# Kernel tuning notes

Hardware: AMD Instinct MI355X
Metric: run time of the kernel (lower is better)

Reference implementation:

```python
import jax, jax.numpy as jnp
import numpy as np

P = 2.0
HARDNESS_RATIO = 0.1
MARGIN = 0.0
EPS = 1e-7

N, DFEAT, NCLS = 4096, 128, 64


def setup_inputs() -> dict:
    key = jax.random.key(0)
    kx, ky = jax.random.split(key)
    x = jax.random.normal(kx, (N, DFEAT), dtype=jnp.float32)
    y = jax.random.randint(ky, (N,), 0, NCLS, dtype=jnp.int64)
    return {"x": x, "y": y}


def reference(x, y):
    # torch.cdist(x, x, p=2) via gram-matrix identity (clamped for sqrt stability)
    sq = jnp.sum(x * x, axis=1)                      # [N]
    D2 = sq[:, None] + sq[None, :] - 2.0 * (x @ x.T)  # [N, N]
    D = jnp.sqrt(jnp.maximum(D2, 1e-12))

    # label agreement masks (no-grad in torch; integer-derived so no float grad anyway)
    agree = (y[None, :] == y[:, None]).astype(x.dtype)   # [N, N]
    disagree = 1.0 - agree
    # With 64 samples/class every row is valid (>=1 positive and >=1 negative),
    # so the torch valid_rows filter keeps all rows; we compute all rows.

    # sort each row by distance, drop self (column 0), gather
    col_idx = jnp.argsort(D, axis=1)[:, 1:]               # [N, N-1]
    dist = jnp.take_along_axis(D, col_idx, axis=1)        # [N, N-1]
    a = jnp.take_along_axis(agree, col_idx, axis=1)
    d = jnp.take_along_axis(disagree, col_idx, axis=1)

    found_agree = jnp.cumsum(a, axis=1)
    found_agree = found_agree / (jnp.sum(found_agree, axis=1, keepdims=True) + EPS)
    found_disagree = jnp.cumsum(d, axis=1)
    found_disagree = found_disagree / (jnp.sum(found_disagree, axis=1, keepdims=True) + EPS)

    negative_hardness = jax.lax.stop_gradient(d * (found_disagree / (found_agree + HARDNESS_RATIO)))
    positive_hardness = jax.lax.stop_gradient(a * ((found_disagree + HARDNESS_RATIO) / (found_agree + HARDNESS_RATIO)))

    per_sample_score = jnp.mean(
        jax.nn.relu(dist * positive_hardness + MARGIN - dist * negative_hardness), axis=1
    )  # [N]

    sample_performance = jnp.sum(found_agree - found_disagree, axis=1)
    sample_performance = sample_performance - jnp.min(sample_performance)
    sample_weight = jax.lax.stop_gradient(1.0 / (sample_performance + 1.0))
    return per_sample_score * sample_weight
```

## Files before the change

### kernel.cpp

```cpp
#include <hip/hip_runtime.h>
#include <math.h>
#include <float.h>


#define N 4096
#define DF 128
#define NCLS 64
#define MAXP 128
#define TSTR 128
#define DSTR 128
#define NB 256
#define HPAD 260
#define BSCALE 0.5f

typedef __bf16 bf16x8 __attribute__((ext_vector_type(8)));
typedef float f32x4 __attribute__((ext_vector_type(4)));
typedef unsigned int u32x4 __attribute__((ext_vector_type(4)));

static __device__ __forceinline__ unsigned short f2bf(float f) {
  unsigned int u = __float_as_uint(f);
  unsigned int r = (u + 0x7fffu + ((u >> 16) & 1u)) >> 16;
  return (unsigned short)r;
}
static __device__ __forceinline__ int d2bin(float d2) {
  int b = (int)(d2 * BSCALE);
  return min(max(b, 0), NB - 1);
}

__global__ void k_prep(const float* __restrict__ x, const int* __restrict__ y,
                       unsigned short* __restrict__ xb, float* __restrict__ sq,
                       unsigned int* __restrict__ cls_cnt, int* __restrict__ cls_idx,
                       int* __restrict__ pos) {
  __shared__ unsigned int c_cnt[NCLS];
  const int tid = threadIdx.x;
  if (blockIdx.x < 1024) {
    const int wave = tid >> 6, lane = tid & 63;
    const int row = (blockIdx.x << 2) + wave;
    const float2 v = *(const float2*)&x[row * DF + (lane << 1)];
    unsigned int b = (unsigned int)f2bf(v.x) | ((unsigned int)f2bf(v.y) << 16);
    *(unsigned int*)&xb[row * DF + (lane << 1)] = b;
    float s = v.x * v.x + v.y * v.y;
    #pragma unroll
    for (int off = 32; off; off >>= 1) s += __shfl_down(s, off);
    if (lane == 0) sq[row] = s;
  } else {
    if (tid < NCLS) c_cnt[tid] = 0u;
    __syncthreads();
    for (int k = tid; k < N; k += 256) {
      const int c = y[k];
      unsigned int p = atomicAdd(&c_cnt[c], 1u);
      if (p >= MAXP) p = MAXP - 1;
      cls_idx[c * MAXP + p] = k;
      pos[k] = (int)p;
    }
    __syncthreads();
    if (tid < NCLS) cls_cnt[tid] = min(c_cnt[tid], (unsigned int)MAXP);
  }
}

__global__ __launch_bounds__(256) void k_gram(
    const unsigned short* __restrict__ xb, const float* __restrict__ sq,
    const unsigned int* __restrict__ cls_cnt, const int* __restrict__ cls_idx,
    float* __restrict__ d2f) {
  __shared__ int plist[MAXP];
  __shared__ float sqL[MAXP];
  const int c = blockIdx.x >> 3;
  const int ti = blockIdx.x & 7;
  const int M = (int)cls_cnt[c];
  const int nT = (M + 15) >> 4;
  if (ti >= nT) return;
  const int tid = threadIdx.x;
  for (int m = tid; m < M; m += 256) {
    const int j = cls_idx[c * MAXP + m];
    plist[m] = j;
    sqL[m] = sq[j];
  }
  __syncthreads();
  const int wave = tid >> 6, lane = tid & 63;
  const int l15 = lane & 15, lg = lane >> 4;
  const int ra = min(ti * 16 + l15, M - 1);
  const u32x4* ap = (const u32x4*)(xb + (size_t)plist[ra] * DF + (lg << 3));
  const bf16x8 a0 = __builtin_bit_cast(bf16x8, ap[0]);
  const bf16x8 a1 = __builtin_bit_cast(bf16x8, ap[4]);
  const bf16x8 a2 = __builtin_bit_cast(bf16x8, ap[8]);
  const bf16x8 a3 = __builtin_bit_cast(bf16x8, ap[12]);
  float sqa[4];
  #pragma unroll
  for (int r = 0; r < 4; ++r) sqa[r] = sqL[min(ti * 16 + lg * 4 + r, M - 1)];
  float* drow = d2f + (size_t)c * (MAXP * DSTR);
  for (int tj = wave; tj < nT; tj += 4) {
    const int rb = min(tj * 16 + l15, M - 1);
    const u32x4* bp = (const u32x4*)(xb + (size_t)plist[rb] * DF + (lg << 3));
    const bf16x8 b0 = __builtin_bit_cast(bf16x8, bp[0]);
    const bf16x8 b1 = __builtin_bit_cast(bf16x8, bp[4]);
    const bf16x8 b2 = __builtin_bit_cast(bf16x8, bp[8]);
    const bf16x8 b3 = __builtin_bit_cast(bf16x8, bp[12]);
    f32x4 acc = {0.f, 0.f, 0.f, 0.f};
    acc = __builtin_amdgcn_mfma_f32_16x16x32_bf16(a0, b0, acc, 0, 0, 0);
    acc = __builtin_amdgcn_mfma_f32_16x16x32_bf16(a1, b1, acc, 0, 0, 0);
    acc = __builtin_amdgcn_mfma_f32_16x16x32_bf16(a2, b2, acc, 0, 0, 0);
    acc = __builtin_amdgcn_mfma_f32_16x16x32_bf16(a3, b3, acc, 0, 0, 0);
    const float sqc = sqL[rb];
    #pragma unroll
    for (int r = 0; r < 4; ++r) {
      const int row = ti * 16 + lg * 4 + r;
      drow[row * DSTR + tj * 16 + l15] = fmaf(-2.0f, acc[r], sqa[r] + sqc);
    }
  }
}

__global__ void k_sort(const int* __restrict__ y, const int* __restrict__ pos,
                       const unsigned int* __restrict__ cls_cnt,
                       const float* __restrict__ d2f, float* __restrict__ thr2,
                       int* __restrict__ Pn, unsigned int* __restrict__ hist) {
  __shared__ float rowL[MAXP];
  const int i = blockIdx.x;
  const int lane = threadIdx.x;
  const u32x4 z = {0u, 0u, 0u, 0u};
  *(u32x4*)&hist[(size_t)i * NB + (lane << 2)] = z;
  const int c = y[i];
  const int rw = pos[i];
  const int M = (int)cls_cnt[c];
  const float* drow = d2f + (size_t)c * (MAXP * DSTR) + (size_t)rw * DSTR;
  rowL[lane] = drow[lane];
  rowL[lane + 64] = drow[lane + 64];
  __syncthreads();
  const float dself = rowL[rw];
  #pragma unroll
  for (int h = 0; h < 2; ++h) {
    const int el = lane + h * 64;
    if (el < M && el != rw) {
      const float dt = rowL[el];
      int r = 0;
      #pragma unroll 4
      for (int s = 0; s < M; ++s) {
        const float ds = rowL[s];
        r += (ds < dt || (ds == dt && s < el)) ? 1 : 0;
      }
      r -= (dself < dt || (dself == dt && rw < el)) ? 1 : 0;
      thr2[(size_t)i * TSTR + r] = dt;
    }
  }
  if (lane == 0) Pn[i] = M - 1;
}

#define ROWS 32
#define CS 8

__global__ __launch_bounds__(256, 4) void k_count(
    const unsigned short* __restrict__ xb, const float* __restrict__ sq,
    unsigned int* __restrict__ hist) {
  __shared__ unsigned int histL[ROWS][HPAD];
  __shared__ float sqcL[512];
  const int rb = blockIdx.x >> 3;
  const int cs = blockIdx.x & 7;
  const int row0 = rb * ROWS;
  const int col0 = cs * 512;
  const int tid = threadIdx.x;
  const int wave = tid >> 6, lane = tid & 63;
  const int l15 = lane & 15, lg = lane >> 4;

  for (int e = tid; e < ROWS * HPAD; e += 256) ((unsigned int*)histL)[e] = 0u;
  if (tid < 256) { sqcL[tid] = sq[col0 + tid]; sqcL[tid + 256] = sq[col0 + 256 + tid]; }

  const u32x4* apA = (const u32x4*)(xb + (size_t)(row0 + l15) * DF + (lg << 3));
  const u32x4* apB = (const u32x4*)(xb + (size_t)(row0 + 16 + l15) * DF + (lg << 3));
  const bf16x8 a0 = __builtin_bit_cast(bf16x8, apA[0]);
  const bf16x8 a1 = __builtin_bit_cast(bf16x8, apA[4]);
  const bf16x8 a2 = __builtin_bit_cast(bf16x8, apA[8]);
  const bf16x8 a3 = __builtin_bit_cast(bf16x8, apA[12]);
  const bf16x8 a4 = __builtin_bit_cast(bf16x8, apB[0]);
  const bf16x8 a5 = __builtin_bit_cast(bf16x8, apB[4]);
  const bf16x8 a6 = __builtin_bit_cast(bf16x8, apB[8]);
  const bf16x8 a7 = __builtin_bit_cast(bf16x8, apB[12]);
  float sqa0[4], sqa1[4];
  #pragma unroll
  for (int r = 0; r < 4; ++r) {
    sqa0[r] = sq[row0 + lg * 4 + r];
    sqa1[r] = sq[row0 + 16 + lg * 4 + r];
  }
  __syncthreads();

  const int jbase = wave * 128;
  #pragma unroll
  for (int t = 0; t < 8; ++t) {
    const int jc = jbase + t * 16;
    const u32x4* bp = (const u32x4*)(xb + (size_t)(col0 + jc + l15) * DF + (lg << 3));
    const bf16x8 b0 = __builtin_bit_cast(bf16x8, bp[0]);
    const bf16x8 b1 = __builtin_bit_cast(bf16x8, bp[4]);
    const bf16x8 b2 = __builtin_bit_cast(bf16x8, bp[8]);
    const bf16x8 b3 = __builtin_bit_cast(bf16x8, bp[12]);
    f32x4 acc0 = {0.f, 0.f, 0.f, 0.f};
    f32x4 acc1 = {0.f, 0.f, 0.f, 0.f};
    acc0 = __builtin_amdgcn_mfma_f32_16x16x32_bf16(a0, b0, acc0, 0, 0, 0);
    acc0 = __builtin_amdgcn_mfma_f32_16x16x32_bf16(a1, b1, acc0, 0, 0, 0);
    acc0 = __builtin_amdgcn_mfma_f32_16x16x32_bf16(a2, b2, acc0, 0, 0, 0);
    acc0 = __builtin_amdgcn_mfma_f32_16x16x32_bf16(a3, b3, acc0, 0, 0, 0);
    acc1 = __builtin_amdgcn_mfma_f32_16x16x32_bf16(a4, b0, acc1, 0, 0, 0);
    acc1 = __builtin_amdgcn_mfma_f32_16x16x32_bf16(a5, b1, acc1, 0, 0, 0);
    acc1 = __builtin_amdgcn_mfma_f32_16x16x32_bf16(a6, b2, acc1, 0, 0, 0);
    acc1 = __builtin_amdgcn_mfma_f32_16x16x32_bf16(a7, b3, acc1, 0, 0, 0);
    const float sqc = sqcL[jc + l15];
    #pragma unroll
    for (int r = 0; r < 4; ++r) {
      const int lr = lg * 4 + r;
      atomicAdd(&histL[lr][d2bin(fmaf(-2.0f, acc0[r], sqa0[r] + sqc))], 1u);
      atomicAdd(&histL[16 + lr][d2bin(fmaf(-2.0f, acc1[r], sqa1[r] + sqc))], 1u);
    }
  }
  __syncthreads();
  for (int e = tid; e < ROWS * NB; e += 256) {
    const unsigned int v = histL[e >> 8][e & 255];
    if (v) atomicAdd(&hist[(size_t)(row0 + (e >> 8)) * NB + (e & 255)], v);
  }
}

__global__ void k_final(const float* __restrict__ thr2, const int* __restrict__ Pn,
                        const unsigned int* __restrict__ hist, float* __restrict__ out) {
  __shared__ unsigned int preL[NB];
  const int i = blockIdx.x;
  const int lane = threadIdx.x;
  const u32x4 h = *(const u32x4*)&hist[(size_t)i * NB + (lane << 2)];
  const unsigned int s0 = h[0], s1 = s0 + h[1], s2 = s1 + h[2], s3 = s2 + h[3];
  unsigned int sc_ = s3;
  #pragma unroll
  for (int off = 1; off < 64; off <<= 1) {
    const unsigned int t = __shfl_up(sc_, off);
    if (lane >= off) sc_ += t;
  }
  const unsigned int base = sc_ - s3;
  preL[(lane << 2) + 0] = base + s0;
  preL[(lane << 2) + 1] = base + s1;
  preL[(lane << 2) + 2] = base + s2;
  preL[(lane << 2) + 3] = base + s3;
  __syncthreads();
  const int P = Pn[i];
  float tv0 = 0.f, tv1 = 0.f;
  int pr0 = 0, pr1 = 0;
  const int r0a = lane, r0b = lane + 64;
  if (r0a < P) {
    tv0 = thr2[(size_t)i * TSTR + r0a];
    pr0 = (int)preL[d2bin(tv0)];
  }
  if (r0b < P) {
    tv1 = thr2[(size_t)i * TSTR + r0b];
    pr1 = (int)preL[d2bin(tv1)];
  }
  int sa = 0;
  if (r0a < P) sa += (N + 1) - pr0;
  if (r0b < P) sa += (N + 1) - pr1;
  #pragma unroll
  for (int off = 32; off; off >>= 1) sa += __shfl_down(sa, off);
  sa = __shfl(sa, 0);
  const float Sa = (float)sa + 1e-7f;
  const float Sd = (float)(8386560 - sa) + 1e-7f;
  float sc = 0.f;
  if (r0a < P) {
    const float fa = (float)(r0a + 1) / Sa;
    const float fd = (float)((pr0 - 1) - (r0a + 1)) / Sd;
    sc += sqrtf(fmaxf(tv0, 1e-12f)) * (fd + 0.1f) / (fa + 0.1f);
  }
  if (r0b < P) {
    const float fa = (float)(r0b + 1) / Sa;
    const float fd = (float)((pr1 - 1) - (r0b + 1)) / Sd;
    sc += sqrtf(fmaxf(tv1, 1e-12f)) * (fd + 0.1f) / (fa + 0.1f);
  }
  #pragma unroll
  for (int off = 32; off; off >>= 1) sc += __shfl_down(sc, off);
  if (lane == 0) out[i] = sc * (1.0f / 4095.0f);
}

extern "C" void kernel_launch(void* const* d_in, const int* in_sizes, int n_in,
                              void* d_out, int out_size, void* d_ws, size_t ws_size,
                              hipStream_t stream) {
  const float* x = (const float*)d_in[0];
  const int* y = (const int*)d_in[1];
  float* out = (float*)d_out;
  char* ws = (char*)d_ws;
  unsigned short* xb    = (unsigned short*)ws;
  float* sq             = (float*)(ws + 1048576);
  int* Pn               = (int*)(ws + 1064960);
  unsigned int* cls_cnt = (unsigned int*)(ws + 1081344);
  int* cls_idx          = (int*)(ws + 1081600);
  int* pos              = (int*)(ws + 1114368);
  float* thr2           = (float*)(ws + 1130752);
  unsigned int* hist    = (unsigned int*)(ws + 3227904);
  float* d2f            = (float*)(ws + 7422208);

  k_prep<<<1025, 256, 0, stream>>>(x, y, xb, sq, cls_cnt, cls_idx, pos);
  k_gram<<<NCLS * 8, 256, 0, stream>>>(xb, sq, cls_cnt, cls_idx, d2f);
  k_sort<<<N, 64, 0, stream>>>(y, pos, cls_cnt, d2f, thr2, Pn, hist);
  k_count<<<(N / ROWS) * CS, 256, 0, stream>>>(xb, sq, hist);
  k_final<<<N, 64, 0, stream>>>(thr2, Pn, hist, out);
}
```

Before: 108.6 us.

## Fuse per-row rank computation into final kernel and zero histogram in prep

Removes the k_sort kernel. Its in-class rank counting now happens inside k_final, which reads the class distance row itself and computes each element's rank directly, so the thr2 scatter buffer and the Pn array are gone. Histogram zeroing moves into k_prep's row blocks. This saves one launch and a global round-trip through thr2, at the cost of a longer serial rank loop inside k_final.

```diff
diff --git a/kernel.cpp b/kernel.cpp
--- a/kernel.cpp
+++ b/kernel.cpp
@@ -7,7 +7,6 @@
 #define DF 128
 #define NCLS 64
 #define MAXP 128
-#define TSTR 128
 #define DSTR 128
 #define NB 256
 #define HPAD 260
@@ -30,7 +29,7 @@
 __global__ void k_prep(const float* __restrict__ x, const int* __restrict__ y,
                        unsigned short* __restrict__ xb, float* __restrict__ sq,
                        unsigned int* __restrict__ cls_cnt, int* __restrict__ cls_idx,
-                       int* __restrict__ pos) {
+                       int* __restrict__ pos, unsigned int* __restrict__ hist) {
   __shared__ unsigned int c_cnt[NCLS];
   const int tid = threadIdx.x;
   if (blockIdx.x < 1024) {
@@ -39,6 +38,8 @@
     const float2 v = *(const float2*)&x[row * DF + (lane << 1)];
     unsigned int b = (unsigned int)f2bf(v.x) | ((unsigned int)f2bf(v.y) << 16);
     *(unsigned int*)&xb[row * DF + (lane << 1)] = b;
+    const u32x4 z = {0u, 0u, 0u, 0u};
+    *(u32x4*)&hist[(size_t)blockIdx.x * 1024 + (tid << 2)] = z;
     float s = v.x * v.x + v.y * v.y;
     #pragma unroll
     for (int off = 32; off; off >>= 1) s += __shfl_down(s, off);
@@ -107,41 +108,6 @@
       drow[row * DSTR + tj * 16 + l15] = fmaf(-2.0f, acc[r], sqa[r] + sqc);
     }
   }
-}
-
-__global__ void k_sort(const int* __restrict__ y, const int* __restrict__ pos,
-                       const unsigned int* __restrict__ cls_cnt,
-                       const float* __restrict__ d2f, float* __restrict__ thr2,
-                       int* __restrict__ Pn, unsigned int* __restrict__ hist) {
-  __shared__ float rowL[MAXP];
-  const int i = blockIdx.x;
-  const int lane = threadIdx.x;
-  const u32x4 z = {0u, 0u, 0u, 0u};
-  *(u32x4*)&hist[(size_t)i * NB + (lane << 2)] = z;
-  const int c = y[i];
-  const int rw = pos[i];
-  const int M = (int)cls_cnt[c];
-  const float* drow = d2f + (size_t)c * (MAXP * DSTR) + (size_t)rw * DSTR;
-  rowL[lane] = drow[lane];
-  rowL[lane + 64] = drow[lane + 64];
-  __syncthreads();
-  const float dself = rowL[rw];
-  #pragma unroll
-  for (int h = 0; h < 2; ++h) {
-    const int el = lane + h * 64;
-    if (el < M && el != rw) {
-      const float dt = rowL[el];
-      int r = 0;
-      #pragma unroll 4
-      for (int s = 0; s < M; ++s) {
-        const float ds = rowL[s];
-        r += (ds < dt || (ds == dt && s < el)) ? 1 : 0;
-      }
-      r -= (dself < dt || (dself == dt && rw < el)) ? 1 : 0;
-      thr2[(size_t)i * TSTR + r] = dt;
-    }
-  }
-  if (lane == 0) Pn[i] = M - 1;
 }
 
 #define ROWS 32
@@ -215,11 +181,21 @@
   }
 }
 
-__global__ void k_final(const float* __restrict__ thr2, const int* __restrict__ Pn,
-                        const unsigned int* __restrict__ hist, float* __restrict__ out) {
+__global__ void k_final(const int* __restrict__ y, const int* __restrict__ pos,
+                        const unsigned int* __restrict__ cls_cnt,
+                        const float* __restrict__ d2f,
+                        const unsigned int* __restrict__ hist,
+                        float* __restrict__ out) {
+  __shared__ float rowL[MAXP];
   __shared__ unsigned int preL[NB];
   const int i = blockIdx.x;
   const int lane = threadIdx.x;
+  const int c = y[i];
+  const int rw = pos[i];
+  const int M = (int)cls_cnt[c];
+  const float* drow = d2f + (size_t)c * (MAXP * DSTR) + (size_t)rw * DSTR;
+  rowL[lane] = drow[lane];
+  rowL[lane + 64] = drow[lane + 64];
   const u32x4 h = *(const u32x4*)&hist[(size_t)i * NB + (lane << 2)];
   const unsigned int s0 = h[0], s1 = s0 + h[1], s2 = s1 + h[2], s3 = s2 + h[3];
   unsigned int sc_ = s3;
@@ -234,36 +210,40 @@
   preL[(lane << 2) + 2] = base + s2;
   preL[(lane << 2) + 3] = base + s3;
   __syncthreads();
-  const int P = Pn[i];
-  float tv0 = 0.f, tv1 = 0.f;
-  int pr0 = 0, pr1 = 0;
-  const int r0a = lane, r0b = lane + 64;
-  if (r0a < P) {
-    tv0 = thr2[(size_t)i * TSTR + r0a];
-    pr0 = (int)preL[d2bin(tv0)];
-  }
-  if (r0b < P) {
-    tv1 = thr2[(size_t)i * TSTR + r0b];
-    pr1 = (int)preL[d2bin(tv1)];
-  }
+  const float dself = rowL[rw];
+  const int el0 = lane, el1 = lane + 64;
+  const bool v0 = (el0 < M) && (el0 != rw);
+  const bool v1 = (el1 < M) && (el1 != rw);
+  const float dt0 = v0 ? rowL[el0] : 0.f;
+  const float dt1 = v1 ? rowL[el1] : 0.f;
+  int r0 = 0, r1 = 0;
+  for (int s = 0; s < M; ++s) {
+    const float ds = rowL[s];
+    r0 += (ds < dt0 || (ds == dt0 && s < el0)) ? 1 : 0;
+    r1 += (ds < dt1 || (ds == dt1 && s < el1)) ? 1 : 0;
+  }
+  r0 -= (dself < dt0 || (dself == dt0 && rw < el0)) ? 1 : 0;
+  r1 -= (dself < dt1 || (dself == dt1 && rw < el1)) ? 1 : 0;
+  const int pr0 = v0 ? (int)preL[d2bin(dt0)] : 0;
+  const int pr1 = v1 ? (int)preL[d2bin(dt1)] : 0;
   int sa = 0;
-  if (r0a < P) sa += (N + 1) - pr0;
-  if (r0b < P) sa += (N + 1) - pr1;
+  if (v0) sa += (N + 1) - pr0;
+  if (v1) sa += (N + 1) - pr1;
   #pragma unroll
   for (int off = 32; off; off >>= 1) sa += __shfl_down(sa, off);
   sa = __shfl(sa, 0);
   const float Sa = (float)sa + 1e-7f;
   const float Sd = (float)(8386560 - sa) + 1e-7f;
   float sc = 0.f;
-  if (r0a < P) {
-    const float fa = (float)(r0a + 1) / Sa;
-    const float fd = (float)((pr0 - 1) - (r0a + 1)) / Sd;
-    sc += sqrtf(fmaxf(tv0, 1e-12f)) * (fd + 0.1f) / (fa + 0.1f);
-  }
-  if (r0b < P) {
-    const float fa = (float)(r0b + 1) / Sa;
-    const float fd = (float)((pr1 - 1) - (r0b + 1)) / Sd;
-    sc += sqrtf(fmaxf(tv1, 1e-12f)) * (fd + 0.1f) / (fa + 0.1f);
+  if (v0) {
+    const float fa = (float)(r0 + 1) / Sa;
+    const float fd = (float)((pr0 - 1) - (r0 + 1)) / Sd;
+    sc += sqrtf(fmaxf(dt0, 1e-12f)) * (fd + 0.1f) / (fa + 0.1f);
+  }
+  if (v1) {
+    const float fa = (float)(r1 + 1) / Sa;
+    const float fd = (float)((pr1 - 1) - (r1 + 1)) / Sd;
+    sc += sqrtf(fmaxf(dt1, 1e-12f)) * (fd + 0.1f) / (fa + 0.1f);
   }
   #pragma unroll
   for (int off = 32; off; off >>= 1) sc += __shfl_down(sc, off);
@@ -279,17 +259,14 @@
   char* ws = (char*)d_ws;
   unsigned short* xb    = (unsigned short*)ws;
   float* sq             = (float*)(ws + 1048576);
-  int* Pn               = (int*)(ws + 1064960);
-  unsigned int* cls_cnt = (unsigned int*)(ws + 1081344);
-  int* cls_idx          = (int*)(ws + 1081600);
-  int* pos              = (int*)(ws + 1114368);
-  float* thr2           = (float*)(ws + 1130752);
-  unsigned int* hist    = (unsigned int*)(ws + 3227904);
-  float* d2f            = (float*)(ws + 7422208);
-
-  k_prep<<<1025, 256, 0, stream>>>(x, y, xb, sq, cls_cnt, cls_idx, pos);
+  unsigned int* cls_cnt = (unsigned int*)(ws + 1064960);
+  int* cls_idx          = (int*)(ws + 1065216);
+  int* pos              = (int*)(ws + 1097984);
+  unsigned int* hist    = (unsigned int*)(ws + 1114368);
+  float* d2f            = (float*)(ws + 5308672);
+
+  k_prep<<<1025, 256, 0, stream>>>(x, y, xb, sq, cls_cnt, cls_idx, pos, hist);
   k_gram<<<NCLS * 8, 256, 0, stream>>>(xb, sq, cls_cnt, cls_idx, d2f);
-  k_sort<<<N, 64, 0, stream>>>(y, pos, cls_cnt, d2f, thr2, Pn, hist);
   k_count<<<(N / ROWS) * CS, 256, 0, stream>>>(xb, sq, hist);
-  k_final<<<N, 64, 0, stream>>>(thr2, Pn, hist, out);
-}
+  k_final<<<N, 64, 0, stream>>>(y, pos, cls_cnt, d2f, hist, out);
+}
```

New measurement: 104.7 us. 1.04x faster.
